# Kernel optimization log

Hardware: AMD Instinct MI355X
Metric: run time of the kernel (lower is better)

The kernel has to match this reference:

```python
import jax, jax.numpy as jnp
import numpy as np

EPS = 1e-6
AREA_WIDTH = 3
NHEAD = 8
DIM = 16


def _skew(v):
    # v: [N,3] -> [N,3,3] cross-product matrix
    x, y, z = v[..., 0], v[..., 1], v[..., 2]
    zero = jnp.zeros_like(x)
    return jnp.stack([
        jnp.stack([zero, -z, y], -1),
        jnp.stack([z, zero, -x], -1),
        jnp.stack([-y, x, zero], -1)], -2)


def _create_meshgrid(h, w):
    # kornia create_meshgrid(..., normalized=False): last dim is (x, y), row-major flatten
    xs = jnp.arange(w, dtype=jnp.float32)
    ys = jnp.arange(h, dtype=jnp.float32)
    gx, gy = jnp.meshgrid(xs, ys, indexing='xy')  # [h,w]
    return jnp.stack([gx, gy], -1).reshape(h * w, 2)  # [S,2]


def _epipolar_lines(coord, R, t, K0, K1):
    # coord [S,2]; R [N,3,3]; t [N,3,1] -> lines [N,S,3] (unit-normalized a,b), mode [N,S]
    S = coord.shape[0]
    p = jnp.concatenate([coord, jnp.ones((S, 1), coord.dtype)], -1)  # [S,3]
    E = _skew(t[..., 0]) @ R                                         # [t]_x R
    F = jnp.swapaxes(jnp.linalg.inv(K1), -1, -2) @ E @ jnp.linalg.inv(K0)
    lines = jnp.einsum('nij,sj->nsi', F, p)
    n = jnp.linalg.norm(lines[..., :2], axis=-1, keepdims=True)
    lines = lines / jnp.maximum(n, 1e-12)
    mode = jnp.abs(lines[..., 1]) >= jnp.abs(lines[..., 0])  # True: solve y(x) (|b|>=|a|)
    return lines, mode


def _get_mask(lines, mode, coord, area_width):
    # lines [N,L,3], mode [N,L], coord [S,2] -> within [N,L,S]
    a, b, c = lines[..., 0], lines[..., 1], lines[..., 2]
    xs, ys = coord[:, 0], coord[:, 1]
    hw = area_width / 2.0
    safe = lambda d: jnp.where(jnp.abs(d) < 1e-12, 1e-12, d)
    cy = (-a / safe(b))[..., None] * xs + (-c / safe(b))[..., None]  # [N,L,S]
    cx = (-b / safe(a))[..., None] * ys + (-c / safe(a))[..., None]
    wy = (ys < cy + hw) & (ys > cy - hw)
    wx = (xs < cx + hw) & (xs > cx - hw)
    return jnp.where(mode[..., None], wy, wx)


def _gather_index(within, C):
    # sort-based top-C compaction, index 0 doubles as padding (faithful to source)
    S = within.shape[-1]
    idx = jnp.arange(S, dtype=jnp.int32)
    ti = jnp.where(within, idx[None, None, :], 0)
    ti = jnp.sort(ti, axis=-1)[..., -C:]
    return ti, ti != 0


def _feature_map(x):
    return jax.nn.elu(x) + 1.0


def reference(queries, keys, values, solved_sample, K0, K1, R, t, h0c, w0c, scale):
    N, L, H, D = queries.shape
    sol = np.asarray(solved_sample).astype(bool)  # static split of the batch
    sol_idx = np.nonzero(sol)[0]
    uns_idx = np.nonzero(~sol)[0]
    Q = _feature_map(queries)
    K = _feature_map(keys)
    out = jnp.zeros((N, L, H, D), queries.dtype)

    if sol_idx.size > 0:  # epipolar-gathered candidate attention, direction '0to1'
        coord = _create_meshgrid(h0c, w0c)
        K0s = K0[sol_idx].at[:, :2, :].mul(1.0 / scale)
        K1s = K1[sol_idx].at[:, :2, :].mul(1.0 / scale)
        C = max(h0c, w0c) * AREA_WIDTH
        lines, mode = _epipolar_lines(coord, R[sol_idx], t[sol_idx], K0s, K1s)
        within = _get_mask(lines, mode, coord, AREA_WIDTH)       # [Ns,L,S]
        index, mask = _gather_index(within, C)                    # [Ns,L,C]
        Ns = sol_idx.size
        n_ix = jnp.arange(Ns)[:, None, None]
        Qs = Q[sol_idx]
        Ks = K[sol_idx][n_ix, index]            # [Ns,L,C,H,D]
        Vs = values[sol_idx][n_ix, index]
        m = mask[..., None, None].astype(Ks.dtype)
        Ks = Ks * m
        Vs = Vs * m / C
        KV = jnp.einsum('nlchd,nlchv->nlhdv', Ks, Vs)
        Z = 1.0 / (jnp.einsum('nlhd,nlhd->nlh', Qs, Ks.sum(2)) + EPS)
        out = out.at[sol_idx].set(jnp.einsum('nlhd,nlhdv,nlh->nlhv', Qs, KV, Z) * C)

    if uns_idx.size > 0:  # plain linear attention
        Qu, Ku, Vu = Q[uns_idx], K[uns_idx], values[uns_idx]
        S = Ku.shape[1]
        KV = jnp.einsum('nshd,nshv->nhdv', Ku, Vu / S)
        Z = 1.0 / (jnp.einsum('nlhd,nhd->nlh', Qu, Ku.sum(1)) + EPS)
        out = out.at[uns_idx].set(jnp.einsum('nlhd,nhdv,nlh->nlhv', Qu, KV, Z) * S)
    return out


def setup_inputs() -> dict:
    key = jax.random.key(0)
    kq, kk, kv = jax.random.split(key, 3)
    N, H, D = 4, NHEAD, DIM
    h0c, w0c = 48, 64
    L = h0c * w0c
    queries = jax.random.normal(kq, (N, L, H, D), jnp.float32)
    keys = jax.random.normal(kk, (N, L, H, D), jnp.float32)
    values = jax.random.normal(kv, (N, L, H, D), jnp.float32)
    solved_sample = jnp.array([True, True, False, False])
    Kmat = np.array([[600., 0., 256.], [0., 600., 192.], [0., 0., 1.]], np.float32)
    K0 = jnp.asarray(np.tile(Kmat, (N, 1, 1)))
    Rl, tl = [], []
    for i in range(N):
        th = 0.05 * (i + 1)
        Rl.append(np.array([[np.cos(th), 0., np.sin(th)], [0., 1., 0.],
                            [-np.sin(th), 0., np.cos(th)]], np.float32))
        tl.append(np.array([[0.2 + 0.01 * i], [0.05], [0.02]], np.float32))
    R = jnp.asarray(np.stack(Rl))
    t = jnp.asarray(np.stack(tl))
    return {"queries": queries, "keys": keys, "values": values,
            "solved_sample": solved_sample, "K0": K0, "K1": K0, "R": R, "t": t,
            "h0c": h0c, "w0c": w0c, "scale": 8}
```

## Files before the change

### kernel.cpp

```cpp
#include <hip/hip_runtime.h>
#include <math.h>

#define NHEAD 8
#define DIM   16
#define EPSF  1e-6f
#define KVCH  8

typedef _Float16 half2_t __attribute__((ext_vector_type(2)));
typedef _Float16 half4_t __attribute__((ext_vector_type(4)));

#if defined(__has_builtin)
#if __has_builtin(__builtin_amdgcn_fdot2)
#define HAVE_FDOT2 1
#endif
#endif

__device__ __forceinline__ float dot2(half2_t a, half2_t b, float c) {
#ifdef HAVE_FDOT2
    return __builtin_amdgcn_fdot2(a, b, c, false);
#else
    return c + (float)a.x * (float)b.x + (float)a.y * (float)b.y;
#endif
}

__device__ __forceinline__ float4 f4add(float4 a, float4 b) {
    return make_float4(a.x + b.x, a.y + b.y, a.z + b.z, a.w + b.w);
}

__device__ __forceinline__ bool solved_flag(const void* p, int i) {
    const unsigned int* u = (const unsigned int*)p;
    unsigned int v0 = u[0];
    if (v0 <= 1u)             return u[i] != 0u;
    if (v0 == 0x3F800000u)    return ((const float*)p)[i] != 0.0f;
    return ((const unsigned char*)p)[i] != 0;
}

__device__ __forceinline__ float fm(float x) {
    return x > 0.f ? x + 1.f : expf(x);
}

__device__ void inv3d(const double* M, double* inv) {
    double det = M[0]*(M[4]*M[8]-M[5]*M[7]) - M[1]*(M[3]*M[8]-M[5]*M[6]) + M[2]*(M[3]*M[7]-M[4]*M[6]);
    double id = 1.0 / det;
    inv[0] =  (M[4]*M[8]-M[5]*M[7])*id;
    inv[1] = -(M[1]*M[8]-M[2]*M[7])*id;
    inv[2] =  (M[1]*M[5]-M[2]*M[4])*id;
    inv[3] = -(M[3]*M[8]-M[5]*M[6])*id;
    inv[4] =  (M[0]*M[8]-M[2]*M[6])*id;
    inv[5] = -(M[0]*M[5]-M[2]*M[3])*id;
    inv[6] =  (M[3]*M[7]-M[4]*M[6])*id;
    inv[7] = -(M[0]*M[7]-M[1]*M[6])*id;
    inv[8] =  (M[0]*M[4]-M[1]*M[3])*id;
}

__device__ void compute_F_one(const float* K0, const float* K1, const float* R,
                              const float* t, float invs, float* Fout, int n) {
    double A[9], B[9];
    for (int i = 0; i < 9; ++i) {
        float a = K0[n*9 + i], b = K1[n*9 + i];
        if (i < 6) { a *= invs; b *= invs; }
        A[i] = (double)a; B[i] = (double)b;
    }
    double iA[9], iB[9];
    inv3d(A, iA); inv3d(B, iB);
    double tx = t[n*3+0], ty = t[n*3+1], tz = t[n*3+2];
    double S[9] = {0.0,-tz,ty, tz,0.0,-tx, -ty,tx,0.0};
    double E[9], M[9];
    for (int i = 0; i < 3; ++i)
        for (int j = 0; j < 3; ++j) {
            double s = 0.0;
            for (int k = 0; k < 3; ++k) s += S[i*3+k] * (double)R[n*9 + k*3 + j];
            E[i*3+j] = s;
        }
    for (int i = 0; i < 3; ++i)
        for (int j = 0; j < 3; ++j) {
            double s = 0.0;
            for (int k = 0; k < 3; ++k) s += E[i*3+k] * iA[k*3+j];
            M[i*3+j] = s;
        }
    for (int i = 0; i < 3; ++i)
        for (int j = 0; j < 3; ++j) {
            double s = 0.0;
            for (int k = 0; k < 3; ++k) s += iB[k*3+i] * M[k*3+j];
            Fout[n*9 + i*3 + j] = (float)s;
        }
}

__launch_bounds__(256)
__global__ void prep_kv(const float4* __restrict__ Kr4, const float4* __restrict__ Vr4,
                        _Float16* __restrict__ KVh, int n4,
                        const float* __restrict__ Kr, const float* __restrict__ Vr,
                        const void* __restrict__ flags,
                        float* __restrict__ KVp, float* __restrict__ Ksp,
                        const float* __restrict__ K0, const float* __restrict__ K1,
                        const float* __restrict__ R,  const float* __restrict__ t,
                        const int* __restrict__ scale_p, float* __restrict__ Fout,
                        int N, int L, int PB) {
    if ((int)blockIdx.x < PB) {
        int i = blockIdx.x * 256 + threadIdx.x;
        if (i < n4) {
            float4 k = Kr4[i];
            float4 v = Vr4[i];
            half4_t kh = { (_Float16)fm(k.x), (_Float16)fm(k.y), (_Float16)fm(k.z), (_Float16)fm(k.w) };
            half4_t vh = { (_Float16)v.x, (_Float16)v.y, (_Float16)v.z, (_Float16)v.w };
            int r = i >> 5;
            int w = (i & 31) << 2;
            *(half4_t*)(KVh + (size_t)r * 256 + w)       = kh;
            *(half4_t*)(KVh + (size_t)r * 256 + 128 + w) = vh;
        }
        if (blockIdx.x == 0 && threadIdx.x < (unsigned)N) {
            float invs = 1.0f / (float)(*scale_p);
            compute_F_one(K0, K1, R, t, invs, Fout, threadIdx.x);
        }
    } else {
        int kb = blockIdx.x - PB;
        int chunk = kb & (KVCH - 1);
        int h = (kb >> 3) & 7;
        int n = kb >> 6;
        if (n >= N || solved_flag(flags, n)) return;
        int tdx = threadIdx.x;
        int d = tdx >> 4, v = tdx & 15;
        int rowsPer = (L + KVCH - 1) / KVCH;
        int r0 = chunk * rowsPer;
        int r1 = min(r0 + rowsPer, L);
        const float* Kb = Kr + (size_t)n * L * (NHEAD * DIM) + h * DIM;
        const float* Vb = Vr + (size_t)n * L * (NHEAD * DIM) + h * DIM;
        float acc = 0.f, ks = 0.f;
        #pragma unroll 8
        for (int s = r0; s < r1; ++s) {
            float kd = fm(Kb[(size_t)s * (NHEAD * DIM) + d]);
            float vv = Vb[(size_t)s * (NHEAD * DIM) + v];
            acc += kd * vv;
            ks  += kd;
        }
        KVp[(((size_t)chunk * N + n) * NHEAD + h) * 256 + (d << 4) + v] = acc;
        if (v == 0) Ksp[(((size_t)chunk * N + n) * NHEAD + h) * 16 + d] = ks;
    }
}

struct Buf {
    uint4 kl, kh, vl, vh;
    float msk;
};
union H16 { uint4 u; half2_t h[4]; _Float16 e[8]; };

__device__ __forceinline__ void issue(Buf& b, const char* KVb, int base16,
                                      float slope, float inter, int oo, float c1,
                                      int ob, int outerN, int innerMax, int sI, int sO) {
    int io = ob + oo;
    float fo = (float)io;
    float cc = fmaf(slope, fo, inter);
    float lo = cc - 1.5f;
    float fl = floorf(lo);
    float fi = fl + c1;
    int ii = (int)fi;
    bool val = (io < outerN) & (ii >= 0) & (ii < innerMax) & (fi > lo) & (fi < cc + 1.5f);
    int s2 = ii * sI + io * sO;
    val = val && (s2 != 0);
    int off = ((val ? s2 : 0) << 9) + base16;
    const char* p = KVb + off;
    b.kl = *(const uint4*)(p);
    b.kh = *(const uint4*)(p + 128);
    b.vl = *(const uint4*)(p + 256);
    b.vh = *(const uint4*)(p + 384);
    b.msk = val ? 1.f : 0.f;
}

__device__ __forceinline__ void consume(const Buf& b, const half2_t* ql, const half2_t* qh,
                                        float* aL, float* aH, float& dL, float& dH) {
    H16 k0, k1, v0, v1;
    k0.u = b.kl; k1.u = b.kh; v0.u = b.vl; v1.u = b.vh;
    float sA = 0.f, sB = 0.f;
    #pragma unroll
    for (int i = 0; i < 4; ++i) {
        sA = dot2(ql[i], k0.h[i], sA);
        sB = dot2(qh[i], k1.h[i], sB);
    }
    sA += __shfl_xor(sA, 1);
    sB += __shfl_xor(sB, 1);
    float scL = sA * b.msk;
    float scH = sB * b.msk;
    dL += scL; dH += scH;
    #pragma unroll
    for (int i = 0; i < 8; ++i) {
        aL[i] = fmaf(scL, (float)v0.e[i], aL[i]);
        aH[i] = fmaf(scH, (float)v1.e[i], aH[i]);
    }
}

__launch_bounds__(256)
__global__ void mega(const float* __restrict__ Qr,
                     const _Float16* __restrict__ KVh,
                     const void* __restrict__ flags,  const float* __restrict__ F,
                     const float* __restrict__ KVp,   const float* __restrict__ Ksp,
                     float* __restrict__ outp,
                     const int* __restrict__ h0c_p, const int* __restrict__ w0c_p,
                     int N, int L, int Bs) {
    if ((int)blockIdx.x < Bs) {
        int g  = blockIdx.x & 7;
        int gb = blockIdx.x >> 3;

        int scnt = 0, smap[8];
        for (int i = 0; i < N && i < 8; ++i)
            if (solved_flag(flags, i)) smap[scnt++] = i;
        if (scnt == 0) return;

        int r   = (g * scnt) >> 3;
        int g0  = (r * 8 + scnt - 1) / scnt;
        int ng  = ((r + 1) * 8 + scnt - 1) / scnt - g0;
        int sub = g - g0;
        int n   = smap[r];

        int wv  = threadIdx.x >> 6;
        int lane = threadIdx.x & 63;
        int q = (gb * ng + sub) * 4 + wv;
        if (q >= L) return;
        q = __builtin_amdgcn_readfirstlane(q);
        int qidx = n * L + q;

        int W  = *w0c_p;
        int Hc = *h0c_p;
        float px = (float)(q % W);
        float py = (float)(q / W);

        const float* Fn = F + n * 9;
        float a = Fn[0]*px + Fn[1]*py + Fn[2];
        float b = Fn[3]*px + Fn[4]*py + Fn[5];
        float c = Fn[6]*px + Fn[7]*py + Fn[8];
        float nrm = sqrtf(a*a + b*b);
        float mdiv = fmaxf(nrm, 1e-12f);
        a /= mdiv; b /= mdiv; c /= mdiv;
        bool mode = fabsf(b) >= fabsf(a);

        float slope, inter;
        int outerN, innerMax, sI, sO;
        if (mode) {
            float bs = (fabsf(b) < 1e-12f) ? 1e-12f : b;
            slope = -a / bs; inter = -c / bs;
            outerN = W; innerMax = Hc; sI = W; sO = 1;
        } else {
            float as = (fabsf(a) < 1e-12f) ? 1e-12f : a;
            slope = -b / as; inter = -c / as;
            outerN = Hc; innerMax = W; sI = 1; sO = W;
        }

        int cL   = lane >> 3;
        int sub8 = lane & 7;
        int hL   = sub8 >> 1;
        int dh   = sub8 & 1;
        int base16 = sub8 << 4;

        const float* qbase = Qr + (size_t)qidx * (NHEAD * DIM);
        half2_t ql[4], qh[4];
        {
            const float4* qa = (const float4*)(qbase + hL * DIM + dh * 8);
            float4 a0 = qa[0], a1 = qa[1];
            ql[0] = (half2_t){ (_Float16)fm(a0.x), (_Float16)fm(a0.y) };
            ql[1] = (half2_t){ (_Float16)fm(a0.z), (_Float16)fm(a0.w) };
            ql[2] = (half2_t){ (_Float16)fm(a1.x), (_Float16)fm(a1.y) };
            ql[3] = (half2_t){ (_Float16)fm(a1.z), (_Float16)fm(a1.w) };
            const float4* qb = (const float4*)(qbase + (hL + 4) * DIM + dh * 8);
            float4 b0 = qb[0], b1 = qb[1];
            qh[0] = (half2_t){ (_Float16)fm(b0.x), (_Float16)fm(b0.y) };
            qh[1] = (half2_t){ (_Float16)fm(b0.z), (_Float16)fm(b0.w) };
            qh[2] = (half2_t){ (_Float16)fm(b1.x), (_Float16)fm(b1.y) };
            qh[3] = (half2_t){ (_Float16)fm(b1.z), (_Float16)fm(b1.w) };
        }

        const char* KVb = (const char*)KVh + (size_t)n * L * 512;

        int mm0 = cL, mm1 = 8 + cL, mm2 = 16 + cL;
        int oo0 = mm0 / 3, oo1 = mm1 / 3, oo2 = mm2 / 3;
        float c10 = (float)(1 + (mm0 - 3 * oo0));
        float c11 = (float)(1 + (mm1 - 3 * oo1));
        float c12 = (float)(1 + (mm2 - 3 * oo2));

        int totalC = outerN * 3;
        int NM3 = (totalC + 23) / 24;

        float accL[8], accH[8];
        #pragma unroll
        for (int i = 0; i < 8; ++i) { accL[i] = 0.f; accH[i] = 0.f; }
        float denL = 0.f, denH = 0.f;

        for (int k = 0; k < NM3; ++k) {
            int ob = k << 3;
            Buf A, B, C;
            issue(A, KVb, base16, slope, inter, oo0, c10, ob, outerN, innerMax, sI, sO);
            issue(B, KVb, base16, slope, inter, oo1, c11, ob, outerN, innerMax, sI, sO);
            issue(C, KVb, base16, slope, inter, oo2, c12, ob, outerN, innerMax, sI, sO);
            consume(A, ql, qh, accL, accH, denL, denH);
            consume(B, ql, qh, accL, accH, denL, denH);
            consume(C, ql, qh, accL, accH, denL, denH);
        }

        #pragma unroll
        for (int j = 0; j < 8; ++j) {
            accL[j] += __shfl_xor(accL[j], 8);
            accL[j] += __shfl_xor(accL[j], 16);
            accL[j] += __shfl_xor(accL[j], 32);
            accH[j] += __shfl_xor(accH[j], 8);
            accH[j] += __shfl_xor(accH[j], 16);
            accH[j] += __shfl_xor(accH[j], 32);
        }
        denL += __shfl_xor(denL, 8);
        denL += __shfl_xor(denL, 16);
        denL += __shfl_xor(denL, 32);
        denH += __shfl_xor(denH, 8);
        denH += __shfl_xor(denH, 16);
        denH += __shfl_xor(denH, 32);

        if (lane < 8) {
            float rL = 1.0f / (denL + EPSF);
            float rH = 1.0f / (denH + EPSF);
            float* op = outp + (size_t)qidx * (NHEAD * DIM) + lane * 8;
            float4 o0 = { accL[0]*rL, accL[1]*rL, accL[2]*rL, accL[3]*rL };
            float4 o1 = { accL[4]*rL, accL[5]*rL, accL[6]*rL, accL[7]*rL };
            ((float4*)op)[0] = o0;
            ((float4*)op)[1] = o1;
            float4 o2 = { accH[0]*rH, accH[1]*rH, accH[2]*rH, accH[3]*rH };
            float4 o3 = { accH[4]*rH, accH[5]*rH, accH[6]*rH, accH[7]*rH };
            ((float4*)(op + 64))[0] = o2;
            ((float4*)(op + 64))[1] = o3;
        }
    } else {
        __shared__ float kvf[8 * 264];
        __shared__ float ksf[8 * 17];
        int t  = threadIdx.x;
        int ib = ((int)blockIdx.x - Bs) << 8;
        int ns0 = ib >> 6;
        int n   = ns0 / L;
        int nlast = (ns0 + 3) / L;
        if (n == nlast) {
            if (solved_flag(flags, n)) return;
            const float* KVpn = KVp + (size_t)n * (NHEAD * 256);
            float4 a0 = make_float4(0.f,0.f,0.f,0.f), a1 = make_float4(0.f,0.f,0.f,0.f);
            #pragma unroll
            for (int ch = 0; ch < KVCH; ++ch) {
                const float4* src = (const float4*)(KVpn + (size_t)ch * (N * NHEAD * 256));
                a0 = f4add(a0, src[2*t]);
                a1 = f4add(a1, src[2*t + 1]);
            }
            {
                int e = t << 3, hh = e >> 8, rr = e & 255;
                *(float4*)&kvf[hh * 264 + rr]     = a0;
                *(float4*)&kvf[hh * 264 + rr + 4] = a1;
            }
            if (t < 32) {
                const float* Kspn = Ksp + (size_t)n * (NHEAD * 16);
                float4 s4 = make_float4(0.f,0.f,0.f,0.f);
                #pragma unroll
                for (int ch = 0; ch < KVCH; ++ch)
                    s4 = f4add(s4, *(const float4*)(Kspn + (size_t)ch * (N * NHEAD * 16) + 4*t));
                int e2 = t << 2, h2 = e2 >> 4, d2 = e2 & 15;
                ksf[h2*17 + d2]     = s4.x;
                ksf[h2*17 + d2 + 1] = s4.y;
                ksf[h2*17 + d2 + 2] = s4.z;
                ksf[h2*17 + d2 + 3] = s4.w;
            }
            __syncthreads();
            int p = t & 63, h = p >> 3, v = (p & 7) * 2;
            int ns = ns0 + (t >> 6);
            const float4* q4 = (const float4*)(Qr + (size_t)ns * (NHEAD * DIM) + h * DIM);
            float4 Q0 = q4[0], Q1 = q4[1], Q2 = q4[2], Q3 = q4[3];
            float qd[16] = { fm(Q0.x), fm(Q0.y), fm(Q0.z), fm(Q0.w),
                             fm(Q1.x), fm(Q1.y), fm(Q1.z), fm(Q1.w),
                             fm(Q2.x), fm(Q2.y), fm(Q2.z), fm(Q2.w),
                             fm(Q3.x), fm(Q3.y), fm(Q3.z), fm(Q3.w) };
            const float* kvh_ = &kvf[h * 264 + v];
            const float* ksh_ = &ksf[h * 17];
            float num0 = 0.f, num1 = 0.f, den = 0.f;
            #pragma unroll
            for (int d = 0; d < 16; ++d) {
                float2 kv2 = *(const float2*)(kvh_ + (d << 4));
                num0 += qd[d] * kv2.x;
                num1 += qd[d] * kv2.y;
                den  += qd[d] * ksh_[d];
            }
            float rdiv = 1.0f / (den + EPSF);
            float2 o2 = { num0 * rdiv, num1 * rdiv };
            *(float2*)(outp + (size_t)ns * (NHEAD * DIM) + h * DIM + v) = o2;
        } else {
            long long tot2 = (long long)N * L * NHEAD * DIM / 2;
            long long idx2 = (long long)ib + t;
            if (idx2 >= tot2) return;
            int p = (int)(idx2 & 63);
            int h = p >> 3;
            int v = (p & 7) * 2;
            long long ns = idx2 >> 6;
            int nn = (int)(ns / L);
            if (solved_flag(flags, nn)) return;
            const float* qrow = Qr + ns * (NHEAD * DIM) + h * DIM;
            float num0 = 0.f, num1 = 0.f, den = 0.f;
            #pragma unroll
            for (int d = 0; d < 16; ++d) {
                float qdv = fm(qrow[d]);
                #pragma unroll
                for (int cch = 0; cch < KVCH; ++cch) {
                    const float2 kv2 = *(const float2*)(KVp + (((size_t)cch * N + nn) * NHEAD + h) * 256 + (d << 4) + v);
                    num0 += qdv * kv2.x;
                    num1 += qdv * kv2.y;
                    den  += qdv * Ksp[(((size_t)cch * N + nn) * NHEAD + h) * 16 + d];
                }
            }
            float rdiv = 1.0f / (den + EPSF);
            size_t ob = ns * (NHEAD * DIM) + h * DIM + v;
            outp[ob]     = num0 * rdiv;
            outp[ob + 1] = num1 * rdiv;
        }
    }
}

extern "C" void kernel_launch(void* const* d_in, const int* in_sizes, int n_in,
                              void* d_out, int out_size, void* d_ws, size_t ws_size,
                              hipStream_t stream) {
    const float* Qr   = (const float*)d_in[0];
    const float* Kr   = (const float*)d_in[1];
    const float* Vr   = (const float*)d_in[2];
    const void*  flag = d_in[3];
    const float* K0   = (const float*)d_in[4];
    const float* K1   = (const float*)d_in[5];
    const float* R    = (const float*)d_in[6];
    const float* t    = (const float*)d_in[7];
    const int*   h0c  = (const int*)d_in[8];
    const int*   w0c  = (const int*)d_in[9];
    const int*   scl  = (const int*)d_in[10];

    int N = in_sizes[3];
    int T = in_sizes[0];
    int L = T / (N * NHEAD * DIM);

    _Float16* KVh = (_Float16*)d_ws;
    float* Fm   = (float*)(KVh + (size_t)2 * T);
    float* KVp  = Fm + (size_t)N * 9;
    float* Ksp  = KVp + (size_t)KVCH * N * NHEAD * 256;

    float* outp = (float*)d_out;

    int n4 = T / 4;
    int PB = (n4 + 255) / 256;
    int KB = N * NHEAD * KVCH;
    prep_kv<<<PB + KB, 256, 0, stream>>>((const float4*)Kr, (const float4*)Vr,
                                         KVh, n4, Kr, Vr, flag, KVp, Ksp,
                                         K0, K1, R, t, scl, Fm, N, L, PB);

    int GB = (L + 7) / 8;
    int Bs = 8 * GB;
    long long tot2 = (long long)N * L * NHEAD * DIM / 2;
    int Bu = (int)((tot2 + 255) / 256);
    mega<<<Bs + Bu, 256, 0, stream>>>(Qr, KVh, flag, Fm, KVp, Ksp, outp,
                                      h0c, w0c, N, L, Bs);
}
```

Baseline: 157.1 us.

## Restructure KV prep reduction with cooperative row loads, shuffles and LDS reduce

The per-chunk K^T V accumulation previously had each of 256 threads own one (d,v) output and loop over every row, issuing redundant strided scalar loads. Now each wave takes a quarter of the rows. Each lane loads one K or V element for two rows per step and broadcasts it with wave shuffles, and each lane accumulates four outputs. The four wave partials are then summed through shared memory. This is meant to cut redundant global loads and serial loop length, at the cost of many shuffle instructions and a block barrier.

```diff
diff --git a/kernel.cpp b/kernel.cpp
--- a/kernel.cpp
+++ b/kernel.cpp
@@ -96,6 +96,8 @@
                         const float* __restrict__ R,  const float* __restrict__ t,
                         const int* __restrict__ scale_p, float* __restrict__ Fout,
                         int N, int L, int PB) {
+    __shared__ float kvred[4][256];
+    __shared__ float ksred[4][16];
     if ((int)blockIdx.x < PB) {
         int i = blockIdx.x * 256 + threadIdx.x;
         if (i < n4) {
@@ -118,23 +120,65 @@
         int h = (kb >> 3) & 7;
         int n = kb >> 6;
         if (n >= N || solved_flag(flags, n)) return;
-        int tdx = threadIdx.x;
-        int d = tdx >> 4, v = tdx & 15;
+
+        int wv   = threadIdx.x >> 6;
+        int lane = threadIdx.x & 63;
+
         int rowsPer = (L + KVCH - 1) / KVCH;
         int r0 = chunk * rowsPer;
         int r1 = min(r0 + rowsPer, L);
-        const float* Kb = Kr + (size_t)n * L * (NHEAD * DIM) + h * DIM;
-        const float* Vb = Vr + (size_t)n * L * (NHEAD * DIM) + h * DIM;
-        float acc = 0.f, ks = 0.f;
-        #pragma unroll 8
-        for (int s = r0; s < r1; ++s) {
-            float kd = fm(Kb[(size_t)s * (NHEAD * DIM) + d]);
-            float vv = Vb[(size_t)s * (NHEAD * DIM) + v];
-            acc += kd * vv;
-            ks  += kd;
-        }
-        KVp[(((size_t)chunk * N + n) * NHEAD + h) * 256 + (d << 4) + v] = acc;
-        if (v == 0) Ksp[(((size_t)chunk * N + n) * NHEAD + h) * 16 + d] = ks;
+        int rowsW = ((rowsPer + 7) / 8) * 2;
+        int w0 = r0 + wv * rowsW;
+        int ngroups = rowsW >> 1;
+
+        bool isV = lane >= 32;
+        int srow_off = (lane >> 4) & 1;
+        int elem = lane & 15;
+        const float* bp = (isV ? Vr : Kr) + ((size_t)n * L) * (NHEAD * DIM) + h * DIM + elem;
+
+        int d   = lane >> 2;
+        int vv4 = (lane & 3) << 2;
+
+        float acc0 = 0.f, acc1 = 0.f, acc2 = 0.f, acc3 = 0.f, ks = 0.f;
+
+        #pragma unroll 4
+        for (int g2 = 0; g2 < ngroups; ++g2) {
+            int s = w0 + (g2 << 1) + srow_off;
+            bool valid = s < r1;
+            int sc = valid ? s : r0;
+            float val = bp[(size_t)sc * (NHEAD * DIM)];
+            if (!isV) val = fm(val);
+            val = valid ? val : 0.f;
+            float k0 = __shfl(val, d);
+            float k1 = __shfl(val, 16 + d);
+            float va0 = __shfl(val, 32 + vv4);
+            float va1 = __shfl(val, 33 + vv4);
+            float va2 = __shfl(val, 34 + vv4);
+            float va3 = __shfl(val, 35 + vv4);
+            float vb0 = __shfl(val, 48 + vv4);
+            float vb1 = __shfl(val, 49 + vv4);
+            float vb2 = __shfl(val, 50 + vv4);
+            float vb3 = __shfl(val, 51 + vv4);
+            acc0 = fmaf(k0, va0, acc0); acc0 = fmaf(k1, vb0, acc0);
+            acc1 = fmaf(k0, va1, acc1); acc1 = fmaf(k1, vb1, acc1);
+            acc2 = fmaf(k0, va2, acc2); acc2 = fmaf(k1, vb2, acc2);
+            acc3 = fmaf(k0, va3, acc3); acc3 = fmaf(k1, vb3, acc3);
+            ks += k0 + k1;
+        }
+
+        *(float4*)&kvred[wv][lane << 2] = make_float4(acc0, acc1, acc2, acc3);
+        if ((lane & 3) == 0) ksred[wv][d] = ks;
+        __syncthreads();
+        if (wv == 0) {
+            float4 rsum = f4add(f4add(*(float4*)&kvred[0][lane << 2],
+                                      *(float4*)&kvred[1][lane << 2]),
+                                f4add(*(float4*)&kvred[2][lane << 2],
+                                      *(float4*)&kvred[3][lane << 2]));
+            *(float4*)(KVp + (((size_t)chunk * N + n) * NHEAD + h) * 256 + (lane << 2)) = rsum;
+            if (lane < 16)
+                Ksp[(((size_t)chunk * N + n) * NHEAD + h) * 16 + lane] =
+                    ksred[0][lane] + ksred[1][lane] + ksred[2][lane] + ksred[3][lane];
+        }
     }
 }
 
```

New measurement: 143.1 us, median of 2. 1.1x faster.
